# Kernel tuning notes

Measured on AMD Instinct MI355X. Metric: run time of the kernel, lower is better.

Reference implementation:

```python
import jax, jax.numpy as jnp
import numpy as np

N_ATOMS = 524288
N_FEAT = 128
BATCH_SIZE = 16384


def setup_inputs() -> dict:
    key = jax.random.key(0)
    k1, k2 = jax.random.split(key)
    atom_features = jax.random.normal(k1, (N_ATOMS, N_FEAT), dtype=jnp.float32)
    membership = jnp.sort(
        jax.random.randint(k2, (N_ATOMS,), 0, BATCH_SIZE, dtype=jnp.int32)
    )
    return {
        "atom_features": atom_features,
        "membership": membership,
        "batch_size": BATCH_SIZE,
    }


def reference(atom_features, membership, batch_size):
    # Fused equivalent of dynamic_partition + per-segment reduce_sum + concat:
    # a single segment-sum keyed on membership. Activation is 'linear' (identity).
    mol_features = jax.ops.segment_sum(
        atom_features, membership, num_segments=batch_size
    )  # (batch_size, n_feat)
    return mol_features
```

## Files before the change

### kernel.cpp

```cpp
#include <hip/hip_runtime.h>

#define N_FEAT 128
#define F4 (N_FEAT / 4)
#define SEGS_PER_BLOCK 4

typedef float vfloat4 __attribute__((ext_vector_type(4)));

__global__ __launch_bounds__(256) void seg_starts_kernel(
    const int* __restrict__ membership, int* __restrict__ starts, int n_atoms,
    int batch)
{
    int i = blockIdx.x * blockDim.x + threadIdx.x;
    if (i >= n_atoms) return;
    int cur  = membership[i];
    int prev = (i == 0) ? -1 : membership[i - 1];
    for (int s = prev + 1; s <= cur; ++s) starts[s] = i;
    if (i == n_atoms - 1) {
        for (int s = cur + 1; s <= batch; ++s) starts[s] = n_atoms;
    }
}

__global__ __launch_bounds__(256) void seg_sum_kernel(
    const float* __restrict__ feats,
    const int* __restrict__ starts,
    float* __restrict__ out,
    int batch)
{
    const int wave = threadIdx.x >> 6;
    const int lane = threadIdx.x & 63;
    const int seg  = blockIdx.x * SEGS_PER_BLOCK + wave;
    if (seg >= batch) return;

    const int lo = starts[seg];
    const int hi = starts[seg + 1];

    const int tx = lane & 31;
    const int ty = lane >> 5;

    const vfloat4* __restrict__ f4 = (const vfloat4*)feats;

    vfloat4 a0 = {0.f, 0.f, 0.f, 0.f};
    vfloat4 a1 = a0, a2 = a0, a3 = a0;

    int r = lo + ty;
    for (; r + 6 < hi; r += 8) {
        const vfloat4* p = f4 + r * F4 + tx;
        vfloat4 v0 = __builtin_nontemporal_load(p);
        vfloat4 v1 = __builtin_nontemporal_load(p + 2 * F4);
        vfloat4 v2 = __builtin_nontemporal_load(p + 4 * F4);
        vfloat4 v3 = __builtin_nontemporal_load(p + 6 * F4);
        a0 += v0;
        a1 += v1;
        a2 += v2;
        a3 += v3;
    }
    for (; r < hi; r += 2) {
        a0 += __builtin_nontemporal_load(f4 + r * F4 + tx);
    }

    vfloat4 acc = (a0 + a1) + (a2 + a3);

    acc.x += __shfl_down(acc.x, 32);
    acc.y += __shfl_down(acc.y, 32);
    acc.z += __shfl_down(acc.z, 32);
    acc.w += __shfl_down(acc.w, 32);

    if (ty == 0) {
        ((vfloat4*)out)[seg * F4 + tx] = acc;
    }
}

extern "C" void kernel_launch(void* const* d_in, const int* in_sizes, int n_in,
                              void* d_out, int out_size, void* d_ws, size_t ws_size,
                              hipStream_t stream) {
    const float* feats      = (const float*)d_in[0];
    const int*   membership = (const int*)d_in[1];
    float*       out        = (float*)d_out;
    int*         starts     = (int*)d_ws;

    const int n_atoms = in_sizes[1];
    const int batch   = out_size / N_FEAT;

    seg_starts_kernel<<<(n_atoms + 255) / 256, 256, 0, stream>>>(
        membership, starts, n_atoms, batch);

    seg_sum_kernel<<<(batch + SEGS_PER_BLOCK - 1) / SEGS_PER_BLOCK, 256, 0,
                     stream>>>(feats, starts, out, batch);
}
```

Baseline: 341.3 us.

## Fuse segment boundary computation into sum kernel via per-wave binary search

Removes the separate kernel that scattered segment start offsets into workspace. Each wave instead binary-searches the sorted membership array for its segment's lower and upper bounds (two lanes, one search each) and broadcasts them by shuffle. This drops one kernel launch, its full pass over membership, and the workspace round trip. In exchange every wave pays about 19 dependent global loads of latency before streaming its rows.

```diff
diff --git a/kernel.cpp b/kernel.cpp
--- a/kernel.cpp
+++ b/kernel.cpp
@@ -6,33 +6,29 @@
 
 typedef float vfloat4 __attribute__((ext_vector_type(4)));
 
-__global__ __launch_bounds__(256) void seg_starts_kernel(
-    const int* __restrict__ membership, int* __restrict__ starts, int n_atoms,
-    int batch)
-{
-    int i = blockIdx.x * blockDim.x + threadIdx.x;
-    if (i >= n_atoms) return;
-    int cur  = membership[i];
-    int prev = (i == 0) ? -1 : membership[i - 1];
-    for (int s = prev + 1; s <= cur; ++s) starts[s] = i;
-    if (i == n_atoms - 1) {
-        for (int s = cur + 1; s <= batch; ++s) starts[s] = n_atoms;
-    }
-}
-
-__global__ __launch_bounds__(256) void seg_sum_kernel(
+__global__ __launch_bounds__(256) void seg_sum_fused_kernel(
     const float* __restrict__ feats,
-    const int* __restrict__ starts,
+    const int* __restrict__ membership,
     float* __restrict__ out,
-    int batch)
+    int n_atoms, int batch)
 {
     const int wave = threadIdx.x >> 6;
     const int lane = threadIdx.x & 63;
     const int seg  = blockIdx.x * SEGS_PER_BLOCK + wave;
     if (seg >= batch) return;
 
-    const int lo = starts[seg];
-    const int hi = starts[seg + 1];
+    int res = 0;
+    if (lane < 2) {
+        const int target = seg + lane;
+        int l = 0, r = n_atoms;
+        while (l < r) {
+            int m = (l + r) >> 1;
+            if (membership[m] < target) l = m + 1; else r = m;
+        }
+        res = l;
+    }
+    const int lo = __shfl(res, 0);
+    const int hi = __shfl(res, 1);
 
     const int tx = lane & 31;
     const int ty = lane >> 5;
@@ -76,14 +72,10 @@
     const float* feats      = (const float*)d_in[0];
     const int*   membership = (const int*)d_in[1];
     float*       out        = (float*)d_out;
-    int*         starts     = (int*)d_ws;
 
     const int n_atoms = in_sizes[1];
     const int batch   = out_size / N_FEAT;
 
-    seg_starts_kernel<<<(n_atoms + 255) / 256, 256, 0, stream>>>(
-        membership, starts, n_atoms, batch);
-
-    seg_sum_kernel<<<(batch + SEGS_PER_BLOCK - 1) / SEGS_PER_BLOCK, 256, 0,
-                     stream>>>(feats, starts, out, batch);
+    seg_sum_fused_kernel<<<(batch + SEGS_PER_BLOCK - 1) / SEGS_PER_BLOCK, 256,
+                           0, stream>>>(feats, membership, out, n_atoms, batch);
 }
```

New measurement: 351.6 us. 3.0% more time.
